# Kernel optimization log

Hardware: AMD Instinct MI355X
Metric: run time of the kernel (lower is better)

## Reference

```python
import jax, jax.numpy as jnp
import numpy as np

N = 8192
IN_F = 128
OUT_F = 64
ALPHA = 0.2  # LeakyReLU negative slope
NEG_INF = -1.0e9


def setup_inputs() -> dict:
    key = jax.random.key(0)
    k_x, k_adj, k_W, k_a = jax.random.split(key, 4)
    x = jax.random.normal(k_x, (N, IN_F), dtype=jnp.float32)
    adj = (jax.random.uniform(k_adj, (N, N)) < 0.02).astype(jnp.float32)
    adj = jnp.maximum(adj, jnp.eye(N, dtype=jnp.float32))
    W = jax.random.normal(k_W, (IN_F, OUT_F), dtype=jnp.float32) * (1.414 / np.sqrt(IN_F))
    a = jax.random.normal(k_a, (2 * OUT_F, 1), dtype=jnp.float32) * 0.1
    return {"x": x, "adj": adj, "W": W, "a": a}


def reference(x, adj, W, a):
    # h: [N, out_f]
    h = x @ W
    # GAT scores: e_ij = leakyrelu(a1.h_i + a2.h_j), dense [N, N]
    h_i = h @ a[:OUT_F]            # [N, 1]
    h_j = h @ a[OUT_F:]            # [N, 1]
    e = h_i + h_j.T                # [N, N]
    e = jax.nn.leaky_relu(e, negative_slope=ALPHA)
    # mask non-edges (adj <= 0) with -1e9, then row softmax
    attn_logits = jnp.where(adj > 0, e, NEG_INF)
    attn = jax.nn.softmax(attn_logits, axis=-1)
    # weighted aggregate + ELU (dropout is identity at p=0 / eval)
    out = jax.nn.elu(attn @ h)
    return out
```

## Files before the change

### kernel.cpp

```cpp
#include <hip/hip_runtime.h>
#include <hip/hip_bf16.h>

#define N_NODES 8192
#define IN_F 128
#define OUT_F 64
#define ALPHA 0.2f
#define CAP 1024

__global__ __launch_bounds__(256) void gat_h(
    const float* __restrict__ x, const float* __restrict__ W,
    const float* __restrict__ a, float* __restrict__ h,
    float* __restrict__ hi, float* __restrict__ hj) {
  __shared__ float sW[IN_F * OUT_F];
  int tid = threadIdx.x;
  for (int i = tid; i < IN_F * OUT_F; i += 256) sW[i] = W[i];
  __syncthreads();

  int f = tid & 63;
  int rloc = tid >> 6;
  float a1 = a[f], a2 = a[OUT_F + f];
  int row0 = blockIdx.x * 32;

  for (int rr = 0; rr < 8; ++rr) {
    int row = row0 + rr * 4 + rloc;
    const float4* xr = (const float4*)(x + (size_t)row * IN_F);
    float acc = 0.f;
#pragma unroll
    for (int k4 = 0; k4 < IN_F / 4; ++k4) {
      float4 xv = xr[k4];
      acc = fmaf(xv.x, sW[(k4 * 4 + 0) * 64 + f], acc);
      acc = fmaf(xv.y, sW[(k4 * 4 + 1) * 64 + f], acc);
      acc = fmaf(xv.z, sW[(k4 * 4 + 2) * 64 + f], acc);
      acc = fmaf(xv.w, sW[(k4 * 4 + 3) * 64 + f], acc);
    }
    h[(size_t)row * 64 + f] = acc;
    float vi = acc * a1, vj = acc * a2;
#pragma unroll
    for (int o = 32; o >= 1; o >>= 1) {
      vi += __shfl_xor(vi, o);
      vj += __shfl_xor(vj, o);
    }
    if (f == 0) { hi[row] = vi; hj[row] = vj; }
  }
}

__global__ __launch_bounds__(256) void gat_row(
    const float* __restrict__ adj, const float* __restrict__ h,
    const float* __restrict__ hi, const float* __restrict__ hj,
    float* __restrict__ out) {
  __shared__ int s_idx[CAP + 64];
  __shared__ float s_w[CAP + 64];
  __shared__ int s_cnt;
  __shared__ float s_redA[4];
  __shared__ float s_redB[4];
  __shared__ float s_part[4][64];

  int tid = threadIdx.x;
  int lane = tid & 63;
  int wid = tid >> 6;
  int row = blockIdx.x;

  if (tid == 0) s_cnt = 0;

  const float4* arow = (const float4*)(adj + (size_t)row * N_NODES);
  unsigned int mask = 0;
#pragma unroll
  for (int it = 0; it < 8; ++it) {
    float4 vv = arow[tid + it * 256];
    mask |= (unsigned int)(vv.x > 0.f) << (it * 4 + 0);
    mask |= (unsigned int)(vv.y > 0.f) << (it * 4 + 1);
    mask |= (unsigned int)(vv.z > 0.f) << (it * 4 + 2);
    mask |= (unsigned int)(vv.w > 0.f) << (it * 4 + 3);
  }
  int c = __popc(mask);

  int incl = c;
#pragma unroll
  for (int o = 1; o < 64; o <<= 1) {
    int t = __shfl_up(incl, o);
    if (lane >= o) incl += t;
  }

  __syncthreads();
  int base = 0;
  if (lane == 63) base = atomicAdd(&s_cnt, incl);
  base = __shfl(base, 63);
  int off = base + incl - c;

  float hii = hi[row];
  float lmax = -1e30f;
  unsigned int m = mask;
  while (m) {
    int b = __ffs(m) - 1;
    m &= m - 1;
    int j = ((tid + ((b >> 2) << 8)) << 2) + (b & 3);
    float l = hii + hj[j];
    l = (l > 0.f) ? l : ALPHA * l;
    s_w[off] = l;
    s_idx[off] = j;
    ++off;
    lmax = fmaxf(lmax, l);
  }

#pragma unroll
  for (int o = 32; o >= 1; o >>= 1) lmax = fmaxf(lmax, __shfl_xor(lmax, o));
  if (lane == 0) s_redA[wid] = lmax;
  __syncthreads();
  float bmax = fmaxf(fmaxf(s_redA[0], s_redA[1]), fmaxf(s_redA[2], s_redA[3]));
  int cnt = s_cnt;
  int cnt_pad = (cnt + 15) & ~15;

  float lsum = 0.f;
  for (int e = tid; e < cnt; e += 256) {
    float w = __expf(s_w[e] - bmax);
    s_w[e] = w;
    lsum += w;
  }
  for (int e = cnt + tid; e < cnt_pad; e += 256) {
    s_w[e] = 0.f;
    s_idx[e] = 0;
  }
#pragma unroll
  for (int o = 32; o >= 1; o >>= 1) lsum += __shfl_xor(lsum, o);
  if (lane == 0) s_redB[wid] = lsum;
  __syncthreads();
  float bsum = s_redB[0] + s_redB[1] + s_redB[2] + s_redB[3];

  int f = lane;
  float acc0 = 0.f, acc1 = 0.f, acc2 = 0.f, acc3 = 0.f;
  for (int e = wid * 4; e < cnt_pad; e += 16) {
    int4 id = *(const int4*)&s_idx[e];
    float4 wv = *(const float4*)&s_w[e];
    acc0 = fmaf(wv.x, h[(size_t)id.x * 64 + f], acc0);
    acc1 = fmaf(wv.y, h[(size_t)id.y * 64 + f], acc1);
    acc2 = fmaf(wv.z, h[(size_t)id.z * 64 + f], acc2);
    acc3 = fmaf(wv.w, h[(size_t)id.w * 64 + f], acc3);
  }
  s_part[wid][f] = (acc0 + acc1) + (acc2 + acc3);
  __syncthreads();
  if (tid < 64) {
    float vv = s_part[0][f] + s_part[1][f] + s_part[2][f] + s_part[3][f];
    vv /= bsum;
    vv = (vv > 0.f) ? vv : expm1f(vv);
    out[(size_t)row * 64 + f] = vv;
  }
}

extern "C" void kernel_launch(void* const* d_in, const int* in_sizes, int n_in,
                              void* d_out, int out_size, void* d_ws, size_t ws_size,
                              hipStream_t stream) {
  const float* x   = (const float*)d_in[0];
  const float* adj = (const float*)d_in[1];
  const float* W   = (const float*)d_in[2];
  const float* a   = (const float*)d_in[3];
  float* out = (float*)d_out;

  float* h  = (float*)d_ws;
  float* hi = h + (size_t)N_NODES * OUT_F;
  float* hj = hi + N_NODES;

  gat_h<<<N_NODES / 32, 256, 0, stream>>>(x, W, a, h, hi, hj);
  gat_row<<<N_NODES, 256, 0, stream>>>(adj, h, hi, hj, out);
}
```

Baseline: 83.82 us.

## Process one adjacency row per wavefront and transpose W in shared memory

The row kernel now assigns one adjacency row to each 64-lane wavefront instead of one row per 256-thread block. This removes all block-level syncthreads, the shared atomic and the cross-wave reductions, and gathers neighbors with 8 independent accumulators. The projection kernel stores W transposed with padding so each lane reads float4 weights, and it launches more, smaller blocks. The per-row neighbor cap drops to 512 and entries beyond it are silently truncated, which is safe only because rows hold about 165 edges.

Result: slower. 101.0 us (+20.5%).

```diff
diff --git a/kernel.cpp b/kernel.cpp
--- a/kernel.cpp
+++ b/kernel.cpp
@@ -5,74 +5,78 @@
 #define IN_F 128
 #define OUT_F 64
 #define ALPHA 0.2f
-#define CAP 1024
+#define CAP 512
+#define WT_STRIDE 132
 
-__global__ __launch_bounds__(256) void gat_h(
+__global__ __launch_bounds__(256, 4) void gat_h(
     const float* __restrict__ x, const float* __restrict__ W,
     const float* __restrict__ a, float* __restrict__ h,
     float* __restrict__ hi, float* __restrict__ hj) {
-  __shared__ float sW[IN_F * OUT_F];
+  __shared__ float sWt[OUT_F][WT_STRIDE];
   int tid = threadIdx.x;
-  for (int i = tid; i < IN_F * OUT_F; i += 256) sW[i] = W[i];
+  for (int i = tid; i < IN_F * OUT_F; i += 256) {
+    int k = i >> 6, f = i & 63;
+    sWt[f][k] = W[i];
+  }
   __syncthreads();
 
-  int f = tid & 63;
-  int rloc = tid >> 6;
-  float a1 = a[f], a2 = a[OUT_F + f];
-  int row0 = blockIdx.x * 32;
+  int lane = tid & 63;
+  int wid = tid >> 6;
+  float a1 = a[lane], a2 = a[OUT_F + lane];
+  int row0 = blockIdx.x * 8;
 
-  for (int rr = 0; rr < 8; ++rr) {
-    int row = row0 + rr * 4 + rloc;
+  for (int rr = 0; rr < 2; ++rr) {
+    int row = row0 + rr * 4 + wid;
     const float4* xr = (const float4*)(x + (size_t)row * IN_F);
     float acc = 0.f;
 #pragma unroll
     for (int k4 = 0; k4 < IN_F / 4; ++k4) {
       float4 xv = xr[k4];
-      acc = fmaf(xv.x, sW[(k4 * 4 + 0) * 64 + f], acc);
-      acc = fmaf(xv.y, sW[(k4 * 4 + 1) * 64 + f], acc);
-      acc = fmaf(xv.z, sW[(k4 * 4 + 2) * 64 + f], acc);
-      acc = fmaf(xv.w, sW[(k4 * 4 + 3) * 64 + f], acc);
+      float4 wv = *(const float4*)&sWt[lane][k4 * 4];
+      acc = fmaf(xv.x, wv.x, acc);
+      acc = fmaf(xv.y, wv.y, acc);
+      acc = fmaf(xv.z, wv.z, acc);
+      acc = fmaf(xv.w, wv.w, acc);
     }
-    h[(size_t)row * 64 + f] = acc;
+    h[(size_t)row * 64 + lane] = acc;
     float vi = acc * a1, vj = acc * a2;
 #pragma unroll
     for (int o = 32; o >= 1; o >>= 1) {
       vi += __shfl_xor(vi, o);
       vj += __shfl_xor(vj, o);
     }
-    if (f == 0) { hi[row] = vi; hj[row] = vj; }
+    if (lane == 0) { hi[row] = vi; hj[row] = vj; }
   }
 }
 
-__global__ __launch_bounds__(256) void gat_row(
+__global__ __launch_bounds__(256, 4) void gat_row(
     const float* __restrict__ adj, const float* __restrict__ h,
     const float* __restrict__ hi, const float* __restrict__ hj,
     float* __restrict__ out) {
-  __shared__ int s_idx[CAP + 64];
-  __shared__ float s_w[CAP + 64];
-  __shared__ int s_cnt;
-  __shared__ float s_redA[4];
-  __shared__ float s_redB[4];
-  __shared__ float s_part[4][64];
+  __shared__ int s_idx[4][CAP];
+  __shared__ float s_w[4][CAP];
 
   int tid = threadIdx.x;
   int lane = tid & 63;
   int wid = tid >> 6;
-  int row = blockIdx.x;
-
-  if (tid == 0) s_cnt = 0;
+  int row = blockIdx.x * 4 + wid;
 
   const float4* arow = (const float4*)(adj + (size_t)row * N_NODES);
-  unsigned int mask = 0;
+  unsigned int mask[4];
 #pragma unroll
-  for (int it = 0; it < 8; ++it) {
-    float4 vv = arow[tid + it * 256];
-    mask |= (unsigned int)(vv.x > 0.f) << (it * 4 + 0);
-    mask |= (unsigned int)(vv.y > 0.f) << (it * 4 + 1);
-    mask |= (unsigned int)(vv.z > 0.f) << (it * 4 + 2);
-    mask |= (unsigned int)(vv.w > 0.f) << (it * 4 + 3);
+  for (int g = 0; g < 4; ++g) {
+    unsigned int mk = 0;
+#pragma unroll
+    for (int it = 0; it < 8; ++it) {
+      float4 vv = arow[lane + (g * 8 + it) * 64];
+      mk |= (unsigned int)(vv.x > 0.f) << (it * 4 + 0);
+      mk |= (unsigned int)(vv.y > 0.f) << (it * 4 + 1);
+      mk |= (unsigned int)(vv.z > 0.f) << (it * 4 + 2);
+      mk |= (unsigned int)(vv.w > 0.f) << (it * 4 + 3);
+    }
+    mask[g] = mk;
   }
-  int c = __popc(mask);
+  int c = __popc(mask[0]) + __popc(mask[1]) + __popc(mask[2]) + __popc(mask[3]);
 
   int incl = c;
 #pragma unroll
@@ -80,70 +84,64 @@
     int t = __shfl_up(incl, o);
     if (lane >= o) incl += t;
   }
+  int off = incl - c;
+  int cnt = __shfl(incl, 63);
 
-  __syncthreads();
-  int base = 0;
-  if (lane == 63) base = atomicAdd(&s_cnt, incl);
-  base = __shfl(base, 63);
-  int off = base + incl - c;
-
+  int* widx = s_idx[wid];
+  float* ww = s_w[wid];
   float hii = hi[row];
   float lmax = -1e30f;
-  unsigned int m = mask;
-  while (m) {
-    int b = __ffs(m) - 1;
-    m &= m - 1;
-    int j = ((tid + ((b >> 2) << 8)) << 2) + (b & 3);
-    float l = hii + hj[j];
-    l = (l > 0.f) ? l : ALPHA * l;
-    s_w[off] = l;
-    s_idx[off] = j;
-    ++off;
-    lmax = fmaxf(lmax, l);
+#pragma unroll
+  for (int g = 0; g < 4; ++g) {
+    unsigned int m = mask[g];
+    while (m) {
+      int b = __ffs(m) - 1;
+      m &= m - 1;
+      int j = ((lane + ((g * 8 + (b >> 2)) << 6)) << 2) + (b & 3);
+      float l = hii + hj[j];
+      l = (l > 0.f) ? l : ALPHA * l;
+      if (off < CAP) { widx[off] = j; ww[off] = l; }
+      ++off;
+      lmax = fmaxf(lmax, l);
+    }
   }
 
 #pragma unroll
   for (int o = 32; o >= 1; o >>= 1) lmax = fmaxf(lmax, __shfl_xor(lmax, o));
-  if (lane == 0) s_redA[wid] = lmax;
-  __syncthreads();
-  float bmax = fmaxf(fmaxf(s_redA[0], s_redA[1]), fmaxf(s_redA[2], s_redA[3]));
-  int cnt = s_cnt;
-  int cnt_pad = (cnt + 15) & ~15;
+  if (cnt > CAP) cnt = CAP;
+  int cnt_pad = (cnt + 7) & ~7;
 
   float lsum = 0.f;
-  for (int e = tid; e < cnt; e += 256) {
-    float w = __expf(s_w[e] - bmax);
-    s_w[e] = w;
+  for (int e = lane; e < cnt; e += 64) {
+    float w = __expf(ww[e] - lmax);
+    ww[e] = w;
     lsum += w;
   }
-  for (int e = cnt + tid; e < cnt_pad; e += 256) {
-    s_w[e] = 0.f;
-    s_idx[e] = 0;
-  }
+  if (cnt + lane < cnt_pad) { ww[cnt + lane] = 0.f; widx[cnt + lane] = 0; }
 #pragma unroll
   for (int o = 32; o >= 1; o >>= 1) lsum += __shfl_xor(lsum, o);
-  if (lane == 0) s_redB[wid] = lsum;
-  __syncthreads();
-  float bsum = s_redB[0] + s_redB[1] + s_redB[2] + s_redB[3];
+  float inv = 1.f / lsum;
 
-  int f = lane;
   float acc0 = 0.f, acc1 = 0.f, acc2 = 0.f, acc3 = 0.f;
-  for (int e = wid * 4; e < cnt_pad; e += 16) {
-    int4 id = *(const int4*)&s_idx[e];
-    float4 wv = *(const float4*)&s_w[e];
-    acc0 = fmaf(wv.x, h[(size_t)id.x * 64 + f], acc0);
-    acc1 = fmaf(wv.y, h[(size_t)id.y * 64 + f], acc1);
-    acc2 = fmaf(wv.z, h[(size_t)id.z * 64 + f], acc2);
-    acc3 = fmaf(wv.w, h[(size_t)id.w * 64 + f], acc3);
+  float acc4 = 0.f, acc5 = 0.f, acc6 = 0.f, acc7 = 0.f;
+  for (int e = 0; e < cnt_pad; e += 8) {
+    int4 ia = *(const int4*)&widx[e];
+    int4 ib = *(const int4*)&widx[e + 4];
+    float4 wa = *(const float4*)&ww[e];
+    float4 wb = *(const float4*)&ww[e + 4];
+    acc0 = fmaf(wa.x, h[(size_t)ia.x * 64 + lane], acc0);
+    acc1 = fmaf(wa.y, h[(size_t)ia.y * 64 + lane], acc1);
+    acc2 = fmaf(wa.z, h[(size_t)ia.z * 64 + lane], acc2);
+    acc3 = fmaf(wa.w, h[(size_t)ia.w * 64 + lane], acc3);
+    acc4 = fmaf(wb.x, h[(size_t)ib.x * 64 + lane], acc4);
+    acc5 = fmaf(wb.y, h[(size_t)ib.y * 64 + lane], acc5);
+    acc6 = fmaf(wb.z, h[(size_t)ib.z * 64 + lane], acc6);
+    acc7 = fmaf(wb.w, h[(size_t)ib.w * 64 + lane], acc7);
   }
-  s_part[wid][f] = (acc0 + acc1) + (acc2 + acc3);
-  __syncthreads();
-  if (tid < 64) {
-    float vv = s_part[0][f] + s_part[1][f] + s_part[2][f] + s_part[3][f];
-    vv /= bsum;
-    vv = (vv > 0.f) ? vv : expm1f(vv);
-    out[(size_t)row * 64 + f] = vv;
-  }
+  float vv = ((acc0 + acc1) + (acc2 + acc3)) + ((acc4 + acc5) + (acc6 + acc7));
+  vv *= inv;
+  vv = (vv > 0.f) ? vv : expm1f(vv);
+  out[(size_t)row * 64 + lane] = vv;
 }
 
 extern "C" void kernel_launch(void* const* d_in, const int* in_sizes, int n_in,
@@ -159,6 +157,6 @@
   float* hi = h + (size_t)N_NODES * OUT_F;
   float* hj = hi + N_NODES;
 
-  gat_h<<<N_NODES / 32, 256, 0, stream>>>(x, W, a, h, hi, hj);
-  gat_row<<<N_NODES, 256, 0, stream>>>(adj, h, hi, hj, out);
+  gat_h<<<N_NODES / 8, 256, 0, stream>>>(x, W, a, h, hi, hj);
+  gat_row<<<N_NODES / 4, 256, 0, stream>>>(adj, h, hi, hj, out);
 }
```
